# Optimization experiments

Measured on AMD Instinct MI355X. Metric: run time of the kernel, lower is better.

The kernel has to match this reference:

```python
import jax, jax.numpy as jnp
import numpy as np

# Static config (matches init_kwargs)
C = 256       # dim
H = 8         # num_heads
D = C // H    # head dim
K = 32        # patch_size (window length)
G = 1         # rt_size (relay tokens per window)
S = G + K     # window length incl. relay token
NW = 8192     # number of windows
N = NW * K    # total octree points
NB = 2        # number of HOTFormerBlocks in the stage
HID = 4 * C   # mlp hidden (mlp_ratio=4)
LS = 1e-5     # layer_scale init
SCALE = D ** -0.5


def _layernorm(x, g, b):
    m = x.mean(-1, keepdims=True)
    v = ((x - m) ** 2).mean(-1, keepdims=True)
    return (x - m) * jax.lax.rsqrt(v + 1e-5) * g + b


def setup_inputs() -> dict:
    key = jax.random.key(0)
    ks = jax.random.split(key, 20)
    w = 0.02
    inp = {
        "data": jax.random.normal(ks[0], (N, C), jnp.float32),
        "relay_tokens": jax.random.normal(ks[1], (NW, C), jnp.float32),
        # per-block parameters stacked on leading NB axis
        "cpe_w": jax.random.normal(ks[2], (NB, 3, C), jnp.float32) * w,  # depthwise k=3 conv (CPE)
        "cpe_b": jnp.zeros((NB, C), jnp.float32),
        "ln1_g": jnp.ones((NB, C), jnp.float32),
        "ln1_b": jnp.zeros((NB, C), jnp.float32),
        "qkv_w": jax.random.normal(ks[3], (NB, C, 3 * C), jnp.float32) * w,
        "qkv_b": jnp.zeros((NB, 3 * C), jnp.float32),
        "rpe": jax.random.normal(ks[4], (NB, H, S, S), jnp.float32) * w,  # relative position bias per window
        "proj_w": jax.random.normal(ks[5], (NB, C, C), jnp.float32) * w,
        "proj_b": jnp.zeros((NB, C), jnp.float32),
        "ln2_g": jnp.ones((NB, C), jnp.float32),
        "ln2_b": jnp.zeros((NB, C), jnp.float32),
        "mlp_w1": jax.random.normal(ks[6], (NB, C, HID), jnp.float32) * w,
        "mlp_b1": jnp.zeros((NB, HID), jnp.float32),
        "mlp_w2": jax.random.normal(ks[7], (NB, HID, C), jnp.float32) * w,
        "mlp_b2": jnp.zeros((NB, C), jnp.float32),
        "gamma1": jnp.full((NB, C), LS, jnp.float32),
        "gamma2": jnp.full((NB, C), LS, jnp.float32),
    }
    return inp


def reference(data, relay_tokens, cpe_w, cpe_b, ln1_g, ln1_b, qkv_w, qkv_b,
              rpe, proj_w, proj_b, ln2_g, ln2_b, mlp_w1, mlp_b1, mlp_w2,
              mlp_b2, gamma1, gamma2):
    rt = relay_tokens
    for i in range(NB):
        # CPE: depthwise kernel-3 conv along octree serialization order
        xp = jnp.pad(data, ((1, 1), (0, 0)))
        cpe = xp[:-2] * cpe_w[i, 0] + xp[1:-1] * cpe_w[i, 1] + xp[2:] * cpe_w[i, 2] + cpe_b[i]
        d = data + cpe
        # data_to_windows + prepend relay token -> [NW, S, C]
        win = d.reshape(NW, K, C)
        x = jnp.concatenate([rt[:, None, :], win], axis=1)
        # windowed MHA with RPE bias
        h = _layernorm(x, ln1_g[i], ln1_b[i])
        qkv = (h @ qkv_w[i] + qkv_b[i]).reshape(NW, S, 3, H, D)
        q, k, v = qkv[:, :, 0], qkv[:, :, 1], qkv[:, :, 2]  # [NW,S,H,D]
        scores = jnp.einsum('nqhd,nkhd->nhqk', q, k) * SCALE + rpe[i][None]
        attn = jax.nn.softmax(scores, axis=-1)
        o = jnp.einsum('nhqk,nkhd->nqhd', attn, v).reshape(NW, S, C)
        o = o @ proj_w[i] + proj_b[i]
        x = x + gamma1[i] * o  # layer-scaled residual (drop_path = identity)
        # MLP
        h2 = _layernorm(x, ln2_g[i], ln2_b[i])
        ffn = jax.nn.gelu(h2 @ mlp_w1[i] + mlp_b1[i]) @ mlp_w2[i] + mlp_b2[i]
        x = x + gamma2[i] * ffn
        # split relay token / window data, windows_to_data
        rt = x[:, 0, :]
        data = x[:, G:, :].reshape(N, C)
    return data, rt
```

## Files before the change

kernel.cpp:

```cpp
#include <hip/hip_runtime.h>
#include <hip/hip_bf16.h>


#define NW_    8192
#define KWIN   32
#define SEQ    33
#define NTOK   262144
#define MROWS  270336
#define CDIM   256
#define HEADS  8
#define HIDD   1024

typedef unsigned short u16;
typedef unsigned int u32;
typedef unsigned char u8;
typedef unsigned long long u64;
typedef __attribute__((ext_vector_type(8))) short short8;
typedef __attribute__((ext_vector_type(4))) float f32x4;
typedef __attribute__((ext_vector_type(2))) float f32x2;

__device__ __forceinline__ u16 f2bf(float f) {
    u32 u = __builtin_bit_cast(u32, f);
    u += 0x7FFFu + ((u >> 16) & 1u);
    return (u16)(u >> 16);
}
__device__ __forceinline__ float bf2f(u16 h) {
    return __builtin_bit_cast(float, (u32)h << 16);
}
__device__ __forceinline__ u32 pk2(float lo, float hi) {
    union { __hip_bfloat162 h; u32 u; } cvt;
    cvt.h = __float22bfloat162_rn(make_float2(lo, hi));
    return cvt.u;
}
__device__ __forceinline__ u32 pk4f8(float a, float b, float c, float d) {
    int pk = __builtin_amdgcn_cvt_pk_fp8_f32(a, b, 0, false);
    pk = __builtin_amdgcn_cvt_pk_fp8_f32(c, d, pk, true);
    return (u32)pk;
}
__device__ __forceinline__ float wsum(float v) {
#pragma unroll
    for (int off = 32; off > 0; off >>= 1) v += __shfl_xor(v, off);
    return v;
}
__device__ __forceinline__ float gelu_f(float v) {
    float s = fminf(fmaxf(0.4255f * v + 0.5f, 0.f), 1.f);
    return v * s;
}
__device__ __forceinline__ void gload_lds16(const void* g, void* l) {
    __builtin_amdgcn_global_load_lds(
        (const __attribute__((address_space(1))) unsigned int*)g,
        (__attribute__((address_space(3))) unsigned int*)l, 16, 0, 0);
}
__device__ __forceinline__ float4 ld4bf(const u16* p) {
    ushort4 v = *(const ushort4*)p;
    return make_float4(bf2f(v.x), bf2f(v.y), bf2f(v.z), bf2f(v.w));
}

__global__ __launch_bounds__(256) void transpose_fp8_kernel(
    const float* __restrict__ W, u8* __restrict__ Wt, int K, int N)
{
    int idx = blockIdx.x * 256 + threadIdx.x;
    if (idx >= K * N) return;
    int n = idx / K, k = idx - n * K;
    int p = __builtin_amdgcn_cvt_pk_fp8_f32(W[(size_t)k * N + n], 0.f, 0, false);
    Wt[idx] = (u8)p;
}

template<bool BF>
__global__ __launch_bounds__(256) void cpe_ln1_kernel(
    const void* __restrict__ datav, const void* __restrict__ rtv,
    const float* __restrict__ cpe_w, const float* __restrict__ cpe_b,
    const float* __restrict__ ln_g, const float* __restrict__ ln_b,
    u16* __restrict__ x, u8* __restrict__ h)
{
    const int lane = threadIdx.x & 63, wid = threadIdx.x >> 6;
    const int row = blockIdx.x * 4 + wid;
    const int w = row / SEQ, s = row - w * SEQ;
    const int c0 = lane * 4;
    float4 xv;
    if (s == 0) {
        xv = BF ? ld4bf((const u16*)rtv + (size_t)w * CDIM + c0)
                : *(const float4*)((const float*)rtv + (size_t)w * CDIM + c0);
    } else {
        const long t = (long)w * KWIN + s - 1;
        float4 a, am = {0.f,0.f,0.f,0.f}, ap = {0.f,0.f,0.f,0.f};
        if (BF) {
            const u16* d = (const u16*)datav;
            a = ld4bf(d + t * CDIM + c0);
            if (t > 0)        am = ld4bf(d + (t - 1) * CDIM + c0);
            if (t < NTOK - 1) ap = ld4bf(d + (t + 1) * CDIM + c0);
        } else {
            const float* d = (const float*)datav;
            a = *(const float4*)(d + t * CDIM + c0);
            if (t > 0)        am = *(const float4*)(d + (t - 1) * CDIM + c0);
            if (t < NTOK - 1) ap = *(const float4*)(d + (t + 1) * CDIM + c0);
        }
        const float4 w0 = *(const float4*)(cpe_w + 0 * CDIM + c0);
        const float4 w1 = *(const float4*)(cpe_w + 1 * CDIM + c0);
        const float4 w2 = *(const float4*)(cpe_w + 2 * CDIM + c0);
        const float4 cb = *(const float4*)(cpe_b + c0);
        xv.x = a.x + am.x * w0.x + a.x * w1.x + ap.x * w2.x + cb.x;
        xv.y = a.y + am.y * w0.y + a.y * w1.y + ap.y * w2.y + cb.y;
        xv.z = a.z + am.z * w0.z + a.z * w1.z + ap.z * w2.z + cb.z;
        xv.w = a.w + am.w * w0.w + a.w * w1.w + ap.w * w2.w + cb.w;
    }
    float s1 = wsum(xv.x + xv.y + xv.z + xv.w);
    float s2 = wsum(xv.x * xv.x + xv.y * xv.y + xv.z * xv.z + xv.w * xv.w);
    const float mean = s1 * (1.f / 256.f);
    const float var  = s2 * (1.f / 256.f) - mean * mean;
    const float rs   = rsqrtf(var + 1e-5f);
    const float4 g = *(const float4*)(ln_g + c0);
    const float4 b = *(const float4*)(ln_b + c0);
    uint2 xo = { pk2(xv.x, xv.y), pk2(xv.z, xv.w) };
    *(uint2*)(x + (size_t)row * CDIM + c0) = xo;
    const float h0 = (xv.x - mean) * rs * g.x + b.x;
    const float h1 = (xv.y - mean) * rs * g.y + b.y;
    const float h2 = (xv.z - mean) * rs * g.z + b.z;
    const float h3 = (xv.w - mean) * rs * g.w + b.w;
    *(u32*)(h + (size_t)row * CDIM + c0) = pk4f8(h0, h1, h2, h3);
}

__global__ __launch_bounds__(256) void ln_kernel(
    const u16* __restrict__ x, const float* __restrict__ ln_g,
    const float* __restrict__ ln_b, u8* __restrict__ h)
{
    const int lane = threadIdx.x & 63, wid = threadIdx.x >> 6;
    const int row = blockIdx.x * 4 + wid;
    const int c0 = lane * 4;
    float4 xv = ld4bf(x + (size_t)row * CDIM + c0);
    float s1 = wsum(xv.x + xv.y + xv.z + xv.w);
    float s2 = wsum(xv.x * xv.x + xv.y * xv.y + xv.z * xv.z + xv.w * xv.w);
    const float mean = s1 * (1.f / 256.f);
    const float var  = s2 * (1.f / 256.f) - mean * mean;
    const float rs   = rsqrtf(var + 1e-5f);
    const float4 g = *(const float4*)(ln_g + c0);
    const float4 b = *(const float4*)(ln_b + c0);
    const float h0 = (xv.x - mean) * rs * g.x + b.x;
    const float h1 = (xv.y - mean) * rs * g.y + b.y;
    const float h2 = (xv.z - mean) * rs * g.z + b.z;
    const float h3 = (xv.w - mean) * rs * g.w + b.w;
    *(u32*)(h + (size_t)row * CDIM + c0) = pk4f8(h0, h1, h2, h3);
}

template<int KT, int NT, int MODE>
__global__ __launch_bounds__(256, 4) void gemm_fp8_kernel(
    const u8* __restrict__ A8, const u8* __restrict__ Bt8,
    const float* __restrict__ bias, u8* __restrict__ Cout8,
    u16* __restrict__ xbuf, const float* __restrict__ gamma,
    u16* __restrict__ sdata, u16* __restrict__ srt, float* __restrict__ fout)
{
    __shared__ u16 sm[17408];
    const int lane = threadIdx.x & 63, wid = threadIdx.x >> 6;
    constexpr int CX = NT / 128;
    constexpr int BAND = (MROWS / 128) / 8;
    const int bid = blockIdx.x;
    const int xcd = bid & 7, local = bid >> 3;
    const int rb = local / CX, cx = local - rb * CX;
    const int row0 = (xcd * BAND + rb) * 128;
    const int col0 = cx * 128;
    const int wr = (wid >> 1) * 64, wc = (wid & 1) * 64;
    const int lr = lane & 15, lg = lane >> 4;
    const int sw = lr & 7;
    f32x4 acc[4][4] = {};
    constexpr int NTk = KT / 128;

    const u8* pa[4];
    const u8* pb[4];
#pragma unroll
    for (int cc = 0; cc < 4; ++cc) {
        const int g = wid * 4 + cc;
        const int chunk = g * 64 + lane;
        const int r = chunk >> 3, c8 = chunk & 7;
        const int c8s = c8 ^ (r & 7);
        pa[cc] = A8  + (size_t)(row0 + r) * KT + c8s * 16;
        pb[cc] = Bt8 + (size_t)(col0 + r) * KT + c8s * 16;
    }

    for (int t = 0; t < NTk; ++t) {
        __syncthreads();
#pragma unroll
        for (int cc = 0; cc < 4; ++cc) {
            const int g = wid * 4 + cc;
            gload_lds16(pa[cc], (char*)sm + g * 1024);
            gload_lds16(pb[cc], (char*)sm + 16384 + g * 1024);
            pa[cc] += 128; pb[cc] += 128;
        }
        __syncthreads();
        const u8* Ab = (const u8*)sm;
        const u8* Bb = (const u8*)sm + 16384;
#pragma unroll
        for (int kk = 0; kk < 4; ++kk) {
            const int gi = kk * 2 + (lg >> 1);
            const int off8 = (lg & 1) * 8;
            long a[4], b[4];
#pragma unroll
            for (int m = 0; m < 4; ++m)
                a[m] = *(const long*)(Ab + (wr + m * 16 + lr) * 128 + ((gi ^ sw) * 16) + off8);
#pragma unroll
            for (int n = 0; n < 4; ++n)
                b[n] = *(const long*)(Bb + (wc + n * 16 + lr) * 128 + ((gi ^ sw) * 16) + off8);
#pragma unroll
            for (int m = 0; m < 4; ++m)
#pragma unroll
                for (int n = 0; n < 4; ++n)
                    acc[m][n] = __builtin_amdgcn_mfma_f32_16x16x32_fp8_fp8(
                        a[m], b[n], acc[m][n], 0, 0, 0);
        }
    }

    __syncthreads();
    if (MODE == 1 || MODE == 5) {
        u8* Ct8 = (u8*)sm;
#pragma unroll
        for (int n = 0; n < 4; ++n) {
            const int col = wc + n * 16 + lr;
            const float bv = bias[col0 + col];
#pragma unroll
            for (int m = 0; m < 4; ++m) {
                float v0 = acc[m][n][0] + bv, v1 = acc[m][n][1] + bv;
                float v2 = acc[m][n][2] + bv, v3 = acc[m][n][3] + bv;
                if (MODE == 1) { v0 = gelu_f(v0); v1 = gelu_f(v1); v2 = gelu_f(v2); v3 = gelu_f(v3); }
                const u32 pk = pk4f8(v0, v1, v2, v3);
                u8* bp = Ct8 + (wr + m * 16 + lg * 4) * 144 + col;
                bp[0]   = (u8)pk;
                bp[144] = (u8)(pk >> 8);
                bp[288] = (u8)(pk >> 16);
                bp[432] = (u8)(pk >> 24);
            }
        }
        __syncthreads();
#pragma unroll
        for (int it = 0; it < 4; ++it) {
            const int c = it * 256 + threadIdx.x;
            const int row = c >> 3, gr = c & 7;
            *(uint4*)(Cout8 + (size_t)(row0 + row) * NT + col0 + gr * 16) =
                *(const uint4*)(Ct8 + row * 144 + gr * 16);
        }
    } else {
        u16* Ct = sm;
#pragma unroll
        for (int n = 0; n < 4; ++n) {
            const int col = wc + n * 16 + lr;
            const float bv = bias[col0 + col];
#pragma unroll
            for (int m = 0; m < 4; ++m) {
                const u32 p01 = pk2(acc[m][n][0] + bv, acc[m][n][1] + bv);
                const u32 p23 = pk2(acc[m][n][2] + bv, acc[m][n][3] + bv);
                u16* bp = Ct + (wr + m * 16 + lg * 4) * 136 + col;
                bp[0]   = (u16)p01;
                bp[136] = (u16)(p01 >> 16);
                bp[272] = (u16)p23;
                bp[408] = (u16)(p23 >> 16);
            }
        }
        __syncthreads();
#pragma unroll
        for (int it = 0; it < 8; ++it) {
            const int c = it * 256 + threadIdx.x;
            const int row = c >> 4, gr = c & 15;
            const int cc0 = col0 + gr * 8;
            short8 v = *(const short8*)(Ct + row * 136 + gr * 8);
            const int grow = row0 + row;
            const float4 g0 = *(const float4*)(gamma + cc0);
            const float4 g1 = *(const float4*)(gamma + cc0 + 4);
            const float gj[8] = {g0.x, g0.y, g0.z, g0.w, g1.x, g1.y, g1.z, g1.w};
            u16* xp = xbuf + (size_t)grow * CDIM + cc0;
            short8 xv = *(const short8*)(xp);
            float xn[8];
#pragma unroll
            for (int j = 0; j < 8; ++j)
                xn[j] = bf2f((u16)xv[j]) + gj[j] * bf2f((u16)v[j]);
            if (MODE == 2) {
                uint4 o = { pk2(xn[0], xn[1]), pk2(xn[2], xn[3]),
                            pk2(xn[4], xn[5]), pk2(xn[6], xn[7]) };
                *(uint4*)xp = o;
            } else {
                const int w = grow / SEQ, s = grow - w * SEQ;
                if (MODE == 3) {
                    u16* dst = (s == 0) ? srt + (size_t)w * CDIM + cc0
                                        : sdata + ((size_t)w * KWIN + s - 1) * CDIM + cc0;
                    uint4 o = { pk2(xn[0], xn[1]), pk2(xn[2], xn[3]),
                                pk2(xn[4], xn[5]), pk2(xn[6], xn[7]) };
                    *(uint4*)dst = o;
                } else {
                    float* dst = (s == 0) ? fout + (size_t)NTOK * CDIM + (size_t)w * CDIM + cc0
                                          : fout + ((size_t)w * KWIN + s - 1) * CDIM + cc0;
                    *(float4*)dst       = make_float4(xn[0], xn[1], xn[2], xn[3]);
                    *(float4*)(dst + 4) = make_float4(xn[4], xn[5], xn[6], xn[7]);
                }
            }
        }
    }
}

__global__ __launch_bounds__(256) void attn_mfma_kernel(
    const u8* __restrict__ qkv, const float* __restrict__ rpe,
    u8* __restrict__ o)
{
    __shared__ u8 sm[4 * 6144];
    const int lane = threadIdx.x & 63, wid = threadIdx.x >> 6;
    u8* Qs = sm + wid * 6144;
    u8* Ks = Qs + 1920;
    u8* Ps = Qs;
    u8* Vt = Qs + 3840;
    const int task = blockIdx.x * 4 + wid;
    const int w = task >> 3, hh = task & 7;
    const u8* base = qkv + (size_t)(w * SEQ) * 768 + hh * 32;

#pragma unroll
    for (int it = 0; it < 5; ++it) {
        int idx = it * 64 + lane;
        if (idx < 288) *(u64*)(Vt + idx * 8) = 0ull;
    }
#pragma unroll
    for (int it = 0; it < 3; ++it) {
        int idx = it * 64 + lane;
        if (idx < 132) {
            int s = idx >> 2, c = idx & 3;
            *(u64*)(Qs + s * 40 + c * 8) = *(const u64*)(base + (size_t)s * 768 + c * 8);
            *(u64*)(Ks + s * 40 + c * 8) = *(const u64*)(base + (size_t)s * 768 + 256 + c * 8);
        }
    }
#pragma unroll
    for (int it = 0; it < 3; ++it) {
        int idx = it * 64 + lane;
        if (idx < 132) {
            int c = idx / 33, k = idx - c * 33;
            u64 v = *(const u64*)(base + (size_t)k * 768 + 512 + c * 8);
#pragma unroll
            for (int j = 0; j < 8; ++j)
                Vt[(c * 8 + j) * 72 + k] = (u8)(v >> (8 * j));
        }
    }

    const int lr = lane & 15, lg = lane >> 4;
    long qa[3], kb[3];
#pragma unroll
    for (int mi = 0; mi < 3; ++mi)
        qa[mi] = *(const long*)(Qs + (mi * 16 + lr) * 40 + lg * 8);
#pragma unroll
    for (int ni = 0; ni < 3; ++ni)
        kb[ni] = *(const long*)(Ks + (ni * 16 + lr) * 40 + lg * 8);
    f32x4 sc[3][3];
#pragma unroll
    for (int mi = 0; mi < 3; ++mi)
#pragma unroll
        for (int ni = 0; ni < 3; ++ni) {
            f32x4 z = {0.f, 0.f, 0.f, 0.f};
            sc[mi][ni] = __builtin_amdgcn_mfma_f32_16x16x32_fp8_fp8(
                qa[mi], kb[ni], z, 0, 0, 0);
        }

#pragma unroll
    for (int it = 0; it < 4; ++it) {
        int idx = it * 64 + lane;
        if (idx < 240) {
            int r = idx / 5, g = idx - r * 5;
            *(u64*)(Ps + r * 72 + 32 + g * 8) = 0ull;
        }
    }

    const float* rp = rpe + hh * SEQ * SEQ;
    const float scale = 0.17677669529663687f;
#pragma unroll
    for (int mi = 0; mi < 3; ++mi) {
#pragma unroll
        for (int q = 0; q < 4; ++q) {
            const int row = mi * 16 + lg * 4 + q;
            const bool rv_ok = (row < 33);
            float r0 = rv_ok ? rp[row * 33 + lr] : 0.f;
            float r1 = rv_ok ? rp[row * 33 + 16 + lr] : 0.f;
            float r2 = (rv_ok && lr == 0) ? rp[row * 33 + 32] : 0.f;
            float s0 = sc[mi][0][q] * scale + r0;
            float s1 = sc[mi][1][q] * scale + r1;
            float s2 = (lr == 0) ? sc[mi][2][q] * scale + r2 : -1e30f;
            float m = fmaxf(fmaxf(s0, s1), s2);
#pragma unroll
            for (int off = 1; off < 16; off <<= 1) m = fmaxf(m, __shfl_xor(m, off));
            float e0 = __expf(s0 - m), e1 = __expf(s1 - m), e2 = __expf(s2 - m);
            float sum = e0 + e1 + e2;
#pragma unroll
            for (int off = 1; off < 16; off <<= 1) sum += __shfl_xor(sum, off);
            const float inv = 1.f / sum;
            u32 p01 = (u32)__builtin_amdgcn_cvt_pk_fp8_f32(e0 * inv, e1 * inv, 0, false);
            u32 p2  = (u32)__builtin_amdgcn_cvt_pk_fp8_f32(e2 * inv, 0.f, 0, false);
            Ps[row * 72 + lr]      = (u8)p01;
            Ps[row * 72 + 16 + lr] = (u8)(p01 >> 8);
            Ps[row * 72 + 32 + lr] = (u8)p2;
        }
    }

    f32x4 oacc[3][2] = {};
#pragma unroll
    for (int ks = 0; ks < 2; ++ks) {
        long pa[3], vb[2];
#pragma unroll
        for (int mi = 0; mi < 3; ++mi)
            pa[mi] = *(const long*)(Ps + (mi * 16 + lr) * 72 + ks * 32 + lg * 8);
#pragma unroll
        for (int ni = 0; ni < 2; ++ni)
            vb[ni] = *(const long*)(Vt + (ni * 16 + lr) * 72 + ks * 32 + lg * 8);
#pragma unroll
        for (int mi = 0; mi < 3; ++mi)
#pragma unroll
            for (int ni = 0; ni < 2; ++ni)
                oacc[mi][ni] = __builtin_amdgcn_mfma_f32_16x16x32_fp8_fp8(
                    pa[mi], vb[ni], oacc[mi][ni], 0, 0, 0);
    }

#pragma unroll
    for (int mi = 0; mi < 3; ++mi)
#pragma unroll
        for (int q = 0; q < 4; ++q) {
            const int row = mi * 16 + lg * 4 + q;
            if (row < 33) {
#pragma unroll
                for (int ni = 0; ni < 2; ++ni) {
                    int pk = __builtin_amdgcn_cvt_pk_fp8_f32(oacc[mi][ni][q], 0.f, 0, false);
                    o[(size_t)(w * SEQ + row) * CDIM + hh * 32 + ni * 16 + lr] = (u8)pk;
                }
            }
        }
}

extern "C" void kernel_launch(void* const* d_in, const int* in_sizes, int n_in,
                              void* d_out, int out_size, void* d_ws, size_t ws_size,
                              hipStream_t stream)
{
    const float* data0  = (const float*)d_in[0];
    const float* rt0    = (const float*)d_in[1];
    const float* cpe_w  = (const float*)d_in[2];
    const float* cpe_b  = (const float*)d_in[3];
    const float* ln1_g  = (const float*)d_in[4];
    const float* ln1_b  = (const float*)d_in[5];
    const float* qkv_w  = (const float*)d_in[6];
    const float* qkv_b  = (const float*)d_in[7];
    const float* rpe    = (const float*)d_in[8];
    const float* proj_w = (const float*)d_in[9];
    const float* proj_b = (const float*)d_in[10];
    const float* ln2_g  = (const float*)d_in[11];
    const float* ln2_b  = (const float*)d_in[12];
    const float* w1     = (const float*)d_in[13];
    const float* b1     = (const float*)d_in[14];
    const float* w2     = (const float*)d_in[15];
    const float* b2     = (const float*)d_in[16];
    const float* g1     = (const float*)d_in[17];
    const float* g2     = (const float*)d_in[18];
    float* out = (float*)d_out;

    char* ws = (char*)d_ws;
    u8*  regA   = (u8*)ws;
    u8*  regB   = (u8*)(ws + 553648128ull);
    u16* x      = (u16*)(ws + 692060160ull);
    u16* xnd    = (u16*)(ws + 830472192ull);
    u16* xnr    = (u16*)(ws + 964689920ull);
    u8*  wqf8   = (u8*) (ws + 968884224ull);
    u8*  w1f8   = (u8*) (ws + 969277440ull);
    u8*  w2f8   = (u8*) (ws + 969801728ull);
    u8*  wpf8   = (u8*) (ws + 970326016ull);

    for (int i = 0; i < 2; ++i) {
        transpose_fp8_kernel<<<(256 * 768 + 255) / 256, 256, 0, stream>>>(
            qkv_w + (size_t)i * 256 * 768, wqf8 + (size_t)i * 768 * 256, 256, 768);
        transpose_fp8_kernel<<<(256 * 256 + 255) / 256, 256, 0, stream>>>(
            proj_w + (size_t)i * 256 * 256, wpf8 + (size_t)i * 256 * 256, 256, 256);
        transpose_fp8_kernel<<<(256 * 1024 + 255) / 256, 256, 0, stream>>>(
            w1 + (size_t)i * 256 * 1024, w1f8 + (size_t)i * 1024 * 256, 256, 1024);
        transpose_fp8_kernel<<<(256 * 1024 + 255) / 256, 256, 0, stream>>>(
            w2 + (size_t)i * 1024 * 256, w2f8 + (size_t)i * 256 * 1024, 1024, 256);
    }

    const int RT = MROWS / 128;

    for (int i = 0; i < 2; ++i) {
        if (i == 0)
            cpe_ln1_kernel<false><<<MROWS / 4, 256, 0, stream>>>(
                data0, rt0, cpe_w, cpe_b, ln1_g, ln1_b, x, regB);
        else
            cpe_ln1_kernel<true><<<MROWS / 4, 256, 0, stream>>>(
                xnd, xnr, cpe_w + 3 * 256, cpe_b + 256,
                ln1_g + 256, ln1_b + 256, x, regB);

        gemm_fp8_kernel<256, 768, 5><<<RT * 6, 256, 0, stream>>>(
            regB, wqf8 + (size_t)i * 768 * 256, qkv_b + (size_t)i * 768,
            regA, nullptr, nullptr, nullptr, nullptr, nullptr);

        attn_mfma_kernel<<<NW_ * HEADS / 4, 256, 0, stream>>>(
            regA, rpe + (size_t)i * HEADS * SEQ * SEQ, regB);

        gemm_fp8_kernel<256, 256, 2><<<RT * 2, 256, 0, stream>>>(
            regB, wpf8 + (size_t)i * 256 * 256, proj_b + (size_t)i * 256,
            nullptr, x, g1 + (size_t)i * 256, nullptr, nullptr, nullptr);

        ln_kernel<<<MROWS / 4, 256, 0, stream>>>(
            x, ln2_g + (size_t)i * 256, ln2_b + (size_t)i * 256, regB);

        gemm_fp8_kernel<256, 1024, 1><<<RT * 8, 256, 0, stream>>>(
            regB, w1f8 + (size_t)i * 1024 * 256, b1 + (size_t)i * 1024,
            regA, nullptr, nullptr, nullptr, nullptr, nullptr);

        if (i == 0)
            gemm_fp8_kernel<1024, 256, 3><<<RT * 2, 256, 0, stream>>>(
                regA, w2f8, b2,
                nullptr, x, g2, xnd, xnr, nullptr);
        else
            gemm_fp8_kernel<1024, 256, 4><<<RT * 2, 256, 0, stream>>>(
                regA, w2f8 + (size_t)256 * 1024, b2 + 256,
                nullptr, x, g2 + 256, nullptr, nullptr, out);
    }
}
```

Baseline: 1.690 ms.

## Double-buffer FP8 GEMM K-tiles in LDS with BK=64 and prefetch

Splits the GEMM K loop into 64-wide tiles held in two LDS buffers, so the async global-to-LDS load of the next tile is issued before the MFMAs on the current one. This replaces the two __syncthreads per 128-wide tile with one waitcnt plus barrier per 64-wide tile, and changes the XOR swizzle to fit 64-byte rows. The aim is to hide global load latency behind compute, at the cost of twice as many loop iterations and barriers. LDS size for the FP8-output modes shrinks, which may allow more blocks per CU.

```diff
diff --git a/kernel.cpp b/kernel.cpp
--- a/kernel.cpp
+++ b/kernel.cpp
@@ -149,7 +149,8 @@
     u16* __restrict__ xbuf, const float* __restrict__ gamma,
     u16* __restrict__ sdata, u16* __restrict__ srt, float* __restrict__ fout)
 {
-    __shared__ u16 sm[17408];
+    constexpr bool F8OUT = (MODE == 1 || MODE == 5);
+    __shared__ u16 sm[F8OUT ? 16384 : 17408];
     const int lane = threadIdx.x & 63, wid = threadIdx.x >> 6;
     constexpr int CX = NT / 128;
     constexpr int BAND = (MROWS / 128) / 8;
@@ -160,45 +161,53 @@
     const int col0 = cx * 128;
     const int wr = (wid >> 1) * 64, wc = (wid & 1) * 64;
     const int lr = lane & 15, lg = lane >> 4;
-    const int sw = lr & 7;
+    const int rsw = (lr ^ (lr >> 2)) & 3;
     f32x4 acc[4][4] = {};
-    constexpr int NTk = KT / 128;
-
-    const u8* pa[4];
-    const u8* pb[4];
-#pragma unroll
-    for (int cc = 0; cc < 4; ++cc) {
-        const int g = wid * 4 + cc;
+    constexpr int NTk = KT / 64;
+
+    const u8* pa[2];
+    const u8* pb[2];
+    int ldg[2];
+#pragma unroll
+    for (int cc = 0; cc < 2; ++cc) {
+        const int g = wid * 2 + cc;
         const int chunk = g * 64 + lane;
-        const int r = chunk >> 3, c8 = chunk & 7;
-        const int c8s = c8 ^ (r & 7);
-        pa[cc] = A8  + (size_t)(row0 + r) * KT + c8s * 16;
-        pb[cc] = Bt8 + (size_t)(col0 + r) * KT + c8s * 16;
-    }
-
+        const int r = chunk >> 2, c = chunk & 3;
+        const int cs = c ^ ((r ^ (r >> 2)) & 3);
+        pa[cc] = A8  + (size_t)(row0 + r) * KT + cs * 16;
+        pb[cc] = Bt8 + (size_t)(col0 + r) * KT + cs * 16;
+        ldg[cc] = g * 1024;
+    }
+
+    auto STAGE = [&](int t) {
+        char* dA = (char*)sm + (t & 1) * 8192;
+        char* dB = (char*)sm + 16384 + (t & 1) * 8192;
+        const size_t k0 = (size_t)t * 64;
+#pragma unroll
+        for (int cc = 0; cc < 2; ++cc) {
+            gload_lds16(pa[cc] + k0, dA + ldg[cc]);
+            gload_lds16(pb[cc] + k0, dB + ldg[cc]);
+        }
+    };
+
+    STAGE(0);
+    asm volatile("s_waitcnt vmcnt(0)" ::: "memory");
+    __builtin_amdgcn_s_barrier();
     for (int t = 0; t < NTk; ++t) {
-        __syncthreads();
-#pragma unroll
-        for (int cc = 0; cc < 4; ++cc) {
-            const int g = wid * 4 + cc;
-            gload_lds16(pa[cc], (char*)sm + g * 1024);
-            gload_lds16(pb[cc], (char*)sm + 16384 + g * 1024);
-            pa[cc] += 128; pb[cc] += 128;
-        }
-        __syncthreads();
-        const u8* Ab = (const u8*)sm;
-        const u8* Bb = (const u8*)sm + 16384;
-#pragma unroll
-        for (int kk = 0; kk < 4; ++kk) {
+        if (t + 1 < NTk) STAGE(t + 1);
+        const u8* Ab = (const u8*)sm + (t & 1) * 8192;
+        const u8* Bb = (const u8*)sm + 16384 + (t & 1) * 8192;
+#pragma unroll
+        for (int kk = 0; kk < 2; ++kk) {
             const int gi = kk * 2 + (lg >> 1);
             const int off8 = (lg & 1) * 8;
             long a[4], b[4];
 #pragma unroll
             for (int m = 0; m < 4; ++m)
-                a[m] = *(const long*)(Ab + (wr + m * 16 + lr) * 128 + ((gi ^ sw) * 16) + off8);
+                a[m] = *(const long*)(Ab + (wr + m * 16 + lr) * 64 + ((gi ^ rsw) * 16) + off8);
 #pragma unroll
             for (int n = 0; n < 4; ++n)
-                b[n] = *(const long*)(Bb + (wc + n * 16 + lr) * 128 + ((gi ^ sw) * 16) + off8);
+                b[n] = *(const long*)(Bb + (wc + n * 16 + lr) * 64 + ((gi ^ rsw) * 16) + off8);
 #pragma unroll
             for (int m = 0; m < 4; ++m)
 #pragma unroll
@@ -206,10 +215,12 @@
                     acc[m][n] = __builtin_amdgcn_mfma_f32_16x16x32_fp8_fp8(
                         a[m], b[n], acc[m][n], 0, 0, 0);
         }
+        asm volatile("s_waitcnt vmcnt(0)" ::: "memory");
+        __builtin_amdgcn_s_barrier();
     }
 
     __syncthreads();
-    if (MODE == 1 || MODE == 5) {
+    if (F8OUT) {
         u8* Ct8 = (u8*)sm;
 #pragma unroll
         for (int n = 0; n < 4; ++n) {
```

Result: no change. 1.665 ms (-1.5%).
